# Kernel optimization log

Hardware: AMD Instinct MI355X
Metric: run time of the kernel (lower is better)

The kernel has to match this reference:

```python
import jax, jax.numpy as jnp
import numpy as np

IN_FEATURES = 4096
OUT_FEATURES = 11008
GROUP_SIZE = 128
NUM_GROUPS = IN_FEATURES // GROUP_SIZE  # 32


def setup_inputs() -> dict:
    key = jax.random.key(0)
    k1, k2, k3, k4 = jax.random.split(key, 4)
    x = jax.random.normal(k1, (8192, IN_FEATURES), dtype=jnp.float32)
    # packed 4-bit weights: one uint8 byte holds two 4-bit values
    qweight = jax.random.randint(k2, (IN_FEATURES * OUT_FEATURES // 2,), 0, 256, dtype=jnp.int32)
    qzeros = jax.random.randint(k3, (OUT_FEATURES, NUM_GROUPS), 0, 16, dtype=jnp.int32)
    scales = jax.random.uniform(k4, (OUT_FEATURES, NUM_GROUPS), dtype=jnp.float32) * 0.01
    return {"x": x, "qweight": qweight, "qzeros": qzeros, "scales": scales}


def _dequantize(qweight, qzeros, scales):
    # unpack: low nibble first, then high nibble (matches stack([low, high], dim=1).view(-1))
    b = qweight.astype(jnp.int32)
    low = b & 15
    high = (b >> 4) & 15
    w = jnp.stack([low, high], axis=1).reshape(-1)  # [in*out]
    w = w[: OUT_FEATURES * IN_FEATURES].reshape(OUT_FEATURES, IN_FEATURES).astype(jnp.float32)
    # per-group dequant: (w - zero) * scale, groups along in_features
    w = w.reshape(OUT_FEATURES, NUM_GROUPS, GROUP_SIZE)
    w = (w - qzeros[:, :, None].astype(jnp.float32)) * scales[:, :, None]
    return w.reshape(OUT_FEATURES, IN_FEATURES)


def reference(x, qweight, qzeros, scales) -> jnp.ndarray:
    weight = _dequantize(qweight, qzeros, scales).astype(x.dtype)  # [out, in]
    # F.linear(x, W) = x @ W.T
    return jnp.einsum("bi,oi->bo", x, weight)
```

## Files before the change

kernel.cpp:

```cpp
#include <hip/hip_runtime.h>
#include <hip/hip_bf16.h>


#define IN_F   4096
#define OUT_F  11008
#define M_DIM  8192
#define NGROUP 32

typedef __bf16 bf16x8 __attribute__((ext_vector_type(8)));
typedef float  f32x4  __attribute__((ext_vector_type(4)));
typedef unsigned short u16;
typedef u16 u16x8v __attribute__((ext_vector_type(8)));

__device__ __forceinline__ u16 f2bf(float f) {
  union { float f; unsigned u; } v; v.f = f;
  unsigned u = v.u;
  return (u16)((u + 0x7fffu + ((u >> 16) & 1u)) >> 16);
}

__device__ __forceinline__ void gload_lds16(const void* gsrc, void* ldst) {
  __builtin_amdgcn_global_load_lds(
      (const __attribute__((address_space(1))) void*)gsrc,
      (__attribute__((address_space(3))) void*)ldst, 16, 0, 0);
}

__global__ __launch_bounds__(256) void dequant_w(const int* __restrict__ qw,
                                                 const int* __restrict__ qz,
                                                 const float* __restrict__ sc,
                                                 u16* __restrict__ W) {
  const int total = (IN_F / 2) * OUT_F / 4;
  int stride = gridDim.x * blockDim.x;
  for (int idx = blockIdx.x * blockDim.x + threadIdx.x; idx < total; idx += stride) {
    int j = idx << 2;
    int o = j >> 11;
    int g = (j >> 6) & 31;
    float z = (float)qz[(o << 5) + g];
    float s = sc[(o << 5) + g];
    int4 q = ((const int4*)qw)[idx];
    int qs0 = q.x, qs1 = q.y, qs2 = q.z, qs3 = q.w;
    u16x8v w;
    w[0] = f2bf(((float)(qs0 & 15) - z) * s);
    w[1] = f2bf(((float)((qs0 >> 4) & 15) - z) * s);
    w[2] = f2bf(((float)(qs1 & 15) - z) * s);
    w[3] = f2bf(((float)((qs1 >> 4) & 15) - z) * s);
    w[4] = f2bf(((float)(qs2 & 15) - z) * s);
    w[5] = f2bf(((float)((qs2 >> 4) & 15) - z) * s);
    w[6] = f2bf(((float)(qs3 & 15) - z) * s);
    w[7] = f2bf(((float)((qs3 >> 4) & 15) - z) * s);
    ((u16x8v*)W)[idx] = w;
  }
}

__global__ __launch_bounds__(256) void cvt_x(const float* __restrict__ x,
                                             u16* __restrict__ Xb) {
  const int total = M_DIM * IN_F / 8;
  int stride = gridDim.x * blockDim.x;
  for (int idx = blockIdx.x * blockDim.x + threadIdx.x; idx < total; idx += stride) {
    float4 a = ((const float4*)x)[idx * 2];
    float4 b = ((const float4*)x)[idx * 2 + 1];
    u16x8v v;
    v[0] = f2bf(a.x); v[1] = f2bf(a.y); v[2] = f2bf(a.z); v[3] = f2bf(a.w);
    v[4] = f2bf(b.x); v[5] = f2bf(b.y); v[6] = f2bf(b.z); v[7] = f2bf(b.w);
    ((u16x8v*)Xb)[idx] = v;
  }
}


#define BAR       __builtin_amdgcn_s_barrier()
#define SCHED0    __builtin_amdgcn_sched_barrier(0)
#define LGKM0     asm volatile("s_waitcnt lgkmcnt(0)" ::: "memory")
#define LGKM8     asm volatile("s_waitcnt lgkmcnt(8)" ::: "memory")
#define VMCNT0    asm volatile("s_waitcnt vmcnt(0)" ::: "memory")
#define VMCNT4    asm volatile("s_waitcnt vmcnt(4)" ::: "memory")
#define PRIO(p)   __builtin_amdgcn_s_setprio(p)

__global__ __launch_bounds__(512, 1) void gemm256(const u16* __restrict__ A,
                                                  const u16* __restrict__ B,
                                                  float* __restrict__ C) {
  constexpr int K = IN_F, N = OUT_F;
  constexpr int NT = K / 64;
  __shared__ __align__(16) u16 sA[2][256 * 64];
  __shared__ __align__(16) u16 sB[2][256 * 64];

  const int NTN = OUT_F / 256;
  const int NWG = (M_DIM / 256) * NTN;
  int bid = blockIdx.x;
  int wg  = (bid & 7) * (NWG / 8) + (bid >> 3);
  int tm = wg / NTN, tn = wg - tm * NTN;
  int m0 = tm * 256, n0 = tn * 256;

  int tid  = threadIdx.x;
  int lane = tid & 63;
  int wave = tid >> 6;
  int wr = wave >> 2, wc = wave & 3;

  int rstage = tid >> 3;
  int gslot  = ((tid & 7) ^ (rstage & 7)) << 3;
  int ldsoff = rstage * 64 + ((tid & 7) << 3);
  const u16* Ag = A + (size_t)(m0 + rstage) * K + gslot;
  const u16* Bg = B + (size_t)(n0 + rstage) * K + gslot;

#define STAGE_A(cb, h, kt) do {                                   \
    const u16* _g = Ag + (size_t)(h) * 128 * K + (kt) * 64;       \
    u16* _l = sA[cb] + (h) * 128 * 64 + ldsoff;                   \
    gload_lds16(_g, _l);                                          \
    gload_lds16(_g + (size_t)64 * K, _l + 64 * 64);               \
  } while (0)

#define STAGE_B(cb, h, kt) do {                                   \
    const u16* _g = Bg + (size_t)(h) * 128 * K + (kt) * 64;       \
    u16* _l = sB[cb] + (h) * 128 * 64 + ldsoff;                   \
    gload_lds16(_g, _l);                                          \
    gload_lds16(_g + (size_t)64 * K, _l + 64 * 64);               \
  } while (0)

  int q8  = lane >> 4;
  int sl0 = ((q8 ^ (lane & 7)) << 3);
  int sl1 = (((q8 | 4) ^ (lane & 7)) << 3);
  int abase = (wr * 128 + (lane & 15)) * 64;
  int bbase = (wc * 64 + (lane & 15)) * 64;

  bf16x8 a0_[8], a1_[8], b0_[4], b1_[4];
  f32x4 acc[8][4] = {};

#define LDA_H(cb, mh, dst) do {                                   \
    const u16* _p = sA[cb] + abase + (mh) * 4096;                 \
    _Pragma("unroll") for (int mf = 0; mf < 4; mf++) {            \
      dst[mf*2+0] = *(const bf16x8*)(_p + mf * 1024 + sl0);       \
      dst[mf*2+1] = *(const bf16x8*)(_p + mf * 1024 + sl1);       \
    }                                                             \
  } while (0)

#define LDB_H(cb, nh, dst) do {                                   \
    const u16* _p = sB[cb] + bbase + (nh) * 2048;                 \
    _Pragma("unroll") for (int nf = 0; nf < 2; nf++) {            \
      dst[nf*2+0] = *(const bf16x8*)(_p + nf * 1024 + sl0);       \
      dst[nf*2+1] = *(const bf16x8*)(_p + nf * 1024 + sl1);       \
    }                                                             \
  } while (0)

#define QUAD16(aq, bq, mh, nh) do {                                            \
    _Pragma("unroll") for (int mf = 0; mf < 4; mf++)                           \
      _Pragma("unroll") for (int nf = 0; nf < 2; nf++)                         \
        acc[(mh)*4+mf][(nh)*2+nf] = __builtin_amdgcn_mfma_f32_16x16x32_bf16(   \
            aq[mf*2+0], bq[nf*2+0], acc[(mh)*4+mf][(nh)*2+nf], 0, 0, 0);       \
    _Pragma("unroll") for (int mf = 0; mf < 4; mf++)                           \
      _Pragma("unroll") for (int nf = 0; nf < 2; nf++)                         \
        acc[(mh)*4+mf][(nh)*2+nf] = __builtin_amdgcn_mfma_f32_16x16x32_bf16(   \
            aq[mf*2+1], bq[nf*2+1], acc[(mh)*4+mf][(nh)*2+nf], 0, 0, 0);       \
  } while (0)

#define TILE4(c, t) do {                                          \
    int _k1 = ((t) + 1) & (NT - 1), _k2 = ((t) + 2) & (NT - 1);   \
     \
    LDA_H(c, 0, a0_); LDB_H(c, 0, b0_);                           \
    STAGE_A((c) ^ 1, 1, _k1);                                     \
    LGKM8; BAR; LGKM0;                                            \
    PRIO(1); QUAD16(a0_, b0_, 0, 0); PRIO(0); BAR;                \
               \
    LDA_H(c, 1, a1_);                                             \
    STAGE_B((c) ^ 1, 1, _k1);                                     \
    BAR; LGKM0;                                                   \
    PRIO(1); QUAD16(a1_, b0_, 1, 0); PRIO(0); BAR;                \
        \
    LDB_H(c, 1, b1_);                                             \
    STAGE_A(c, 0, _k2);                                           \
    BAR; LGKM0;                                                   \
    PRIO(1); QUAD16(a1_, b1_, 1, 1); PRIO(0); BAR;                \
       \
    STAGE_B(c, 0, _k2);                                           \
    BAR;                                                          \
    PRIO(1); QUAD16(a0_, b1_, 0, 1); PRIO(0);                     \
    VMCNT4; BAR;                                                  \
  } while (0)

  STAGE_A(0, 0, 0); STAGE_A(0, 1, 0);
  STAGE_B(0, 0, 0); STAGE_B(0, 1, 0);
  STAGE_A(1, 0, 1); STAGE_B(1, 0, 1);
  VMCNT4; BAR;
  SCHED0;
  asm volatile("" ::: "memory");

#pragma unroll 1
  for (int t = 0; t < NT; t += 2) {
    TILE4(0, t);
    TILE4(1, t + 1);
  }

  float* Cp = C + (size_t)(m0 + wr * 128 + ((lane >> 4) << 2)) * N
                + n0 + wc * 64 + (lane & 15);
#pragma unroll
  for (int mf = 0; mf < 8; mf++)
#pragma unroll
    for (int nf = 0; nf < 4; nf++)
#pragma unroll
      for (int j = 0; j < 4; j++)
        Cp[(size_t)(mf * 16 + j) * N + nf * 16] = acc[mf][nf][j];
}

__global__ __launch_bounds__(256) void naive_gemm(const float* __restrict__ x,
                                                  const int* __restrict__ qw,
                                                  const int* __restrict__ qz,
                                                  const float* __restrict__ sc,
                                                  float* __restrict__ out) {
  __shared__ float xs[IN_F];
  int m = blockIdx.y;
  int n = blockIdx.x * 256 + threadIdx.x;
  for (int i = threadIdx.x; i < IN_F; i += 256) xs[i] = x[(size_t)m * IN_F + i];
  __syncthreads();
  float acc = 0.f;
  const int* qrow = qw + (size_t)n * (IN_F / 2);
  for (int g = 0; g < NGROUP; g++) {
    float z = (float)qz[n * NGROUP + g];
    float s = sc[n * NGROUP + g];
    for (int t = 0; t < 64; t++) {
      int q = qrow[g * 64 + t];
      acc += xs[g * 128 + 2 * t] * ((float)(q & 15) - z) * s;
      acc += xs[g * 128 + 2 * t + 1] * ((float)((q >> 4) & 15) - z) * s;
    }
  }
  out[(size_t)m * OUT_F + n] = acc;
}

extern "C" void kernel_launch(void* const* d_in, const int* in_sizes, int n_in,
                              void* d_out, int out_size, void* d_ws, size_t ws_size,
                              hipStream_t stream) {
  const float* x  = (const float*)d_in[0];
  const int*   qw = (const int*)d_in[1];
  const int*   qz = (const int*)d_in[2];
  const float* sc = (const float*)d_in[3];
  float* out = (float*)d_out;

  const size_t WBYTES = (size_t)OUT_F * IN_F * 2;
  const size_t XBYTES = (size_t)M_DIM * IN_F * 2;

  if (ws_size >= WBYTES + XBYTES) {
    u16* Wb = (u16*)d_ws;
    u16* Xb = (u16*)((char*)d_ws + WBYTES);
    dequant_w<<<2048, 256, 0, stream>>>(qw, qz, sc, Wb);
    cvt_x<<<2048, 256, 0, stream>>>(x, Xb);
    gemm256<<<(M_DIM / 256) * (OUT_F / 256), 512, 0, stream>>>(Xb, Wb, out);
  } else {
    naive_gemm<<<dim3(OUT_F / 256, M_DIM), 256, 0, stream>>>(x, qw, qz, sc, out);
  }
}
```

Baseline: 774.5 us.

## Replace interleaved four-phase GEMM schedule with simple double-buffered tile loop

Replaces the four-phase per-tile schedule, which interleaved half-tile global-to-LDS staging with quarter MFMA blocks and tracked partial vmcnt/lgkmcnt, with a plain double buffer. Each tile now reads all A/B fragments from LDS, issues the full next-tile A/B staging into the other buffer, runs all MFMAs, then waits for all loads and barriers. This removes several barriers and finer-grained waits per tile. The cost is a shallower prefetch (one tile ahead instead of partly two) and a full vmcnt(0) drain every iteration, which may expose global-load latency.

```diff
diff --git a/kernel.cpp b/kernel.cpp
--- a/kernel.cpp
+++ b/kernel.cpp
@@ -69,9 +69,7 @@
 #define BAR       __builtin_amdgcn_s_barrier()
 #define SCHED0    __builtin_amdgcn_sched_barrier(0)
 #define LGKM0     asm volatile("s_waitcnt lgkmcnt(0)" ::: "memory")
-#define LGKM8     asm volatile("s_waitcnt lgkmcnt(8)" ::: "memory")
 #define VMCNT0    asm volatile("s_waitcnt vmcnt(0)" ::: "memory")
-#define VMCNT4    asm volatile("s_waitcnt vmcnt(4)" ::: "memory")
 #define PRIO(p)   __builtin_amdgcn_s_setprio(p)
 
 __global__ __launch_bounds__(512, 1) void gemm256(const u16* __restrict__ A,
@@ -100,18 +98,19 @@
   const u16* Ag = A + (size_t)(m0 + rstage) * K + gslot;
   const u16* Bg = B + (size_t)(n0 + rstage) * K + gslot;
 
-#define STAGE_A(cb, h, kt) do {                                   \
-    const u16* _g = Ag + (size_t)(h) * 128 * K + (kt) * 64;       \
-    u16* _l = sA[cb] + (h) * 128 * 64 + ldsoff;                   \
-    gload_lds16(_g, _l);                                          \
-    gload_lds16(_g + (size_t)64 * K, _l + 64 * 64);               \
-  } while (0)
-
-#define STAGE_B(cb, h, kt) do {                                   \
-    const u16* _g = Bg + (size_t)(h) * 128 * K + (kt) * 64;       \
-    u16* _l = sB[cb] + (h) * 128 * 64 + ldsoff;                   \
-    gload_lds16(_g, _l);                                          \
-    gload_lds16(_g + (size_t)64 * K, _l + 64 * 64);               \
+#define STAGE_AB(cb, kt) do {                                     \
+    const u16* _ga = Ag + (kt) * 64;                              \
+    const u16* _gb = Bg + (kt) * 64;                              \
+    u16* _la = sA[cb] + ldsoff;                                   \
+    u16* _lb = sB[cb] + ldsoff;                                   \
+    gload_lds16(_ga, _la);                                        \
+    gload_lds16(_ga + (size_t)64 * K, _la + 64 * 64);             \
+    gload_lds16(_ga + (size_t)128 * K, _la + 128 * 64);           \
+    gload_lds16(_ga + (size_t)192 * K, _la + 192 * 64);           \
+    gload_lds16(_gb, _lb);                                        \
+    gload_lds16(_gb + (size_t)64 * K, _lb + 64 * 64);             \
+    gload_lds16(_gb + (size_t)128 * K, _lb + 128 * 64);           \
+    gload_lds16(_gb + (size_t)192 * K, _lb + 192 * 64);           \
   } while (0)
 
   int q8  = lane >> 4;
@@ -150,41 +149,29 @@
             aq[mf*2+1], bq[nf*2+1], acc[(mh)*4+mf][(nh)*2+nf], 0, 0, 0);       \
   } while (0)
 
-#define TILE4(c, t) do {                                          \
-    int _k1 = ((t) + 1) & (NT - 1), _k2 = ((t) + 2) & (NT - 1);   \
-     \
+#define TILE(c, t) do {                                           \
+    int _k1 = ((t) + 1) & (NT - 1);                               \
     LDA_H(c, 0, a0_); LDB_H(c, 0, b0_);                           \
-    STAGE_A((c) ^ 1, 1, _k1);                                     \
-    LGKM8; BAR; LGKM0;                                            \
-    PRIO(1); QUAD16(a0_, b0_, 0, 0); PRIO(0); BAR;                \
-               \
-    LDA_H(c, 1, a1_);                                             \
-    STAGE_B((c) ^ 1, 1, _k1);                                     \
-    BAR; LGKM0;                                                   \
-    PRIO(1); QUAD16(a1_, b0_, 1, 0); PRIO(0); BAR;                \
-        \
-    LDB_H(c, 1, b1_);                                             \
-    STAGE_A(c, 0, _k2);                                           \
-    BAR; LGKM0;                                                   \
-    PRIO(1); QUAD16(a1_, b1_, 1, 1); PRIO(0); BAR;                \
-       \
-    STAGE_B(c, 0, _k2);                                           \
-    BAR;                                                          \
-    PRIO(1); QUAD16(a0_, b1_, 0, 1); PRIO(0);                     \
-    VMCNT4; BAR;                                                  \
-  } while (0)
-
-  STAGE_A(0, 0, 0); STAGE_A(0, 1, 0);
-  STAGE_B(0, 0, 0); STAGE_B(0, 1, 0);
-  STAGE_A(1, 0, 1); STAGE_B(1, 0, 1);
-  VMCNT4; BAR;
+    LDA_H(c, 1, a1_); LDB_H(c, 1, b1_);                           \
+    STAGE_AB((c) ^ 1, _k1);                                       \
+    PRIO(1);                                                      \
+    QUAD16(a0_, b0_, 0, 0);                                       \
+    QUAD16(a0_, b1_, 0, 1);                                       \
+    QUAD16(a1_, b0_, 1, 0);                                       \
+    QUAD16(a1_, b1_, 1, 1);                                       \
+    PRIO(0);                                                      \
+    VMCNT0; LGKM0; BAR;                                           \
+  } while (0)
+
+  STAGE_AB(0, 0);
+  VMCNT0; BAR;
   SCHED0;
   asm volatile("" ::: "memory");
 
 #pragma unroll 1
   for (int t = 0; t < NT; t += 2) {
-    TILE4(0, t);
-    TILE4(1, t + 1);
+    TILE(0, t);
+    TILE(1, t + 1);
   }
 
   float* Cp = C + (size_t)(m0 + wr * 128 + ((lane >> 4) << 2)) * N
```

Result: no change. 773.7 us (-0.1%).
